# Optimization experiments

Measured on AMD Instinct MI355X. Metric: run time of the kernel, lower is better.

## Reference

```python
import jax, jax.numpy as jnp
import numpy as np

N = 100000      # nodes
E = 3200000     # edges
F_IN = 78       # num_features_mol
F_GAT = 256     # mol_out_feats
HEADS = 2
F_HYP = 128     # mol_out_feats_hyper


def setup_inputs() -> dict:
    key = jax.random.key(0)
    ks = jax.random.split(key, 32)
    g = lambda k, s: jax.random.normal(k, s, dtype=jnp.float32) * 0.05
    inp = {}
    inp["mol_x"] = jax.random.normal(ks[0], (N, F_IN), dtype=jnp.float32)
    inp["mol_edge_index"] = jax.random.randint(ks[1], (2, E), 0, N)
    inp["hyper_edge"] = jax.random.randint(ks[2], (2, E), 0, N)
    # GAT layer 1 (78 -> 256, 2 heads, concat=False)
    inp["W1"] = g(ks[3], (F_IN, HEADS * F_GAT)); inp["as1"] = g(ks[4], (HEADS, F_GAT)); inp["ad1"] = g(ks[5], (HEADS, F_GAT)); inp["b1"] = jnp.zeros((F_GAT,), jnp.float32)
    # GAT layers 2,3 (256 -> 256)
    inp["W2"] = g(ks[6], (F_GAT, HEADS * F_GAT)); inp["as2"] = g(ks[7], (HEADS, F_GAT)); inp["ad2"] = g(ks[8], (HEADS, F_GAT)); inp["b2"] = jnp.zeros((F_GAT,), jnp.float32)
    inp["W3"] = g(ks[9], (F_GAT, HEADS * F_GAT)); inp["as3"] = g(ks[10], (HEADS, F_GAT)); inp["ad3"] = g(ks[11], (HEADS, F_GAT)); inp["b3"] = jnp.zeros((F_GAT,), jnp.float32)
    # GRU-style gating fusion
    inp["fc1_w"] = g(ks[12], (F_GAT, F_GAT)); inp["fc1_b"] = jnp.zeros((F_GAT,), jnp.float32)
    inp["fc2_w"] = g(ks[13], (F_GAT, F_GAT)); inp["fc2_b"] = jnp.zeros((F_GAT,), jnp.float32)
    inp["mol_bias"] = jax.random.uniform(ks[14], (1, F_GAT), jnp.float32, -0.2, 0.2)
    # HypergraphConv layers (334 -> 128 -> 128)
    inp["theta1"] = g(ks[15], (F_GAT + F_IN, F_HYP)); inp["hb1"] = jnp.zeros((F_HYP,), jnp.float32)
    inp["theta2"] = g(ks[16], (F_HYP, F_HYP)); inp["hb2"] = jnp.zeros((F_HYP,), jnp.float32)
    return inp


def _gat(x, src, dst, W, a_s, a_d, b):
    # PyG GATConv, heads=2, concat=False, eval mode (no dropout), self-loops pre-added in src/dst
    xh = (x @ W).reshape(N, HEADS, F_GAT)            # [N,H,C]
    a_src = (xh * a_s).sum(-1)                        # [N,H]
    a_dst = (xh * a_d).sum(-1)                        # [N,H]
    e = jax.nn.leaky_relu(a_src[src] + a_dst[dst], 0.2)  # [E',H]
    m = jax.ops.segment_max(e, dst, num_segments=N)
    ex = jnp.exp(e - m[dst])
    s = jax.ops.segment_sum(ex, dst, num_segments=N)
    alpha = ex / s[dst]                               # softmax over incoming edges
    out = jax.ops.segment_sum(xh[src] * alpha[:, :, None], dst, num_segments=N)
    return out.mean(axis=1) + b                       # concat=False -> head mean


def _hyper(x, node, edge, theta, b):
    # PyG HypergraphConv, use_attention=False: D^-1 H B^-1 H^T X Theta + b
    xt = x @ theta
    ones = jnp.ones((node.shape[0],), xt.dtype)
    D = jax.ops.segment_sum(ones, node, num_segments=N)
    B = jax.ops.segment_sum(ones, edge, num_segments=N)
    Dinv = jnp.where(D > 0, 1.0 / D, 0.0)
    Binv = jnp.where(B > 0, 1.0 / B, 0.0)
    ef = Binv[:, None] * jax.ops.segment_sum(xt[node], edge, num_segments=N)
    nf = Dinv[:, None] * jax.ops.segment_sum(ef[edge], node, num_segments=N)
    return nf + b


def _forward(mol_x, mol_edge_index, hyper_edge,
             W1, as1, ad1, b1, W2, as2, ad2, b2, W3, as3, ad3, b3,
             fc1_w, fc1_b, fc2_w, fc2_b, mol_bias, theta1, hb1, theta2, hb2):
    loops = jnp.arange(N, dtype=mol_edge_index.dtype)
    src = jnp.concatenate([mol_edge_index[0], loops])
    dst = jnp.concatenate([mol_edge_index[1], loops])
    hyper_x0 = jax.lax.stop_gradient(mol_x)  # .clone().detach()
    # layer 0
    h = jax.nn.relu(_gat(mol_x, src, dst, W1, as1, ad1, b1))
    # layer 1 (relu) + gate
    x = jax.nn.relu(_gat(h, src, dst, W2, as2, ad2, b2))
    z = jax.nn.sigmoid(x @ fc1_w.T + fc1_b + h @ fc2_w.T + fc2_b + mol_bias)
    h = z * x + (1.0 - z) * h
    # layer 2 (no relu) + gate
    x = _gat(h, src, dst, W3, as3, ad3, b3)
    z = jax.nn.sigmoid(x @ fc1_w.T + fc1_b + h @ fc2_w.T + fc2_b + mol_bias)
    h = z * x + (1.0 - z) * h
    # hypergraph branch (source uses mol_edge_index here, hyper_edge is unused)
    hx = jnp.concatenate([jax.lax.stop_gradient(h), hyper_x0], axis=1)
    node, edge = mol_edge_index[0], mol_edge_index[1]
    hx = jax.nn.relu(_hyper(hx, node, edge, theta1, hb1))
    hx = jax.nn.relu(_hyper(hx, node, edge, theta2, hb2))
    return jnp.concatenate([h, hx], axis=1)  # [N, 384]


def reference(mol_x, mol_edge_index, hyper_edge,
              W1, as1, ad1, b1, W2, as2, ad2, b2, W3, as3, ad3, b3,
              fc1_w, fc1_b, fc2_w, fc2_b, mol_bias, theta1, hb1, theta2, hb2):
    return _forward(mol_x, mol_edge_index, hyper_edge,
                    W1, as1, ad1, b1, W2, as2, ad2, b2, W3, as3, ad3, b3,
                    fc1_w, fc1_b, fc2_w, fc2_b, mol_bias, theta1, hb1, theta2, hb2)
```

## Files before the change

kernel.cpp:

```cpp
#include <hip/hip_runtime.h>

typedef unsigned short u16;
typedef __attribute__((ext_vector_type(8))) short short8v;
typedef __attribute__((ext_vector_type(8))) unsigned short ushort8v;
typedef __attribute__((ext_vector_type(4))) unsigned short ushort4v;
typedef __attribute__((ext_vector_type(4))) float f32x4;
typedef __attribute__((ext_vector_type(2))) float f32x2;

__device__ __forceinline__ float bf2f(u16 u) {
    union { unsigned int i; float f; } v; v.i = ((unsigned int)u) << 16; return v.f;
}
__device__ __forceinline__ u16 f2bf(float f) {
    union { float f; unsigned int i; } v; v.f = f;
    unsigned int i = v.i;
    return (u16)((i + 0x7FFFu + ((i >> 16) & 1u)) >> 16);
}
__device__ __forceinline__ float leaky02(float x) { return x > 0.f ? x : 0.2f * x; }
__device__ __forceinline__ float load_in(const void* p, long i, int isbf) {
    return isbf ? bf2f(((const u16*)p)[i]) : ((const float*)p)[i];
}
__device__ __forceinline__ f32x2 pk_fma(f32x2 a, f32x2 b, f32x2 c) {
    f32x2 d;
    asm("v_pk_fma_f32 %0, %1, %2, %3" : "=v"(d) : "v"(a), "v"(b), "v"(c));
    return d;
}
__device__ __forceinline__ f32x2 pk_add(f32x2 a, f32x2 b) {
    f32x2 d;
    asm("v_pk_add_f32 %0, %1, %2" : "=v"(d) : "v"(a), "v"(b));
    return d;
}
__device__ __forceinline__ f32x2 bfpair(unsigned int d) {
    union { unsigned int i; float f; } lo, hi;
    lo.i = d << 16;
    hi.i = d & 0xFFFF0000u;
    f32x2 r; r.x = lo.f; r.y = hi.f; return r;
}
__device__ __forceinline__ float bperm_f(int addr, float v) {
    return __int_as_float(__builtin_amdgcn_ds_bpermute(addr, __float_as_int(v)));
}
__device__ __forceinline__ int bperm_i(int addr, int v) {
    return __builtin_amdgcn_ds_bpermute(addr, v);
}

__global__ void detect_kernel(const unsigned* __restrict__ w, int* __restrict__ flag) {
    __shared__ int cnt;
    int t = threadIdx.x;
    if (t == 0) cnt = 0;
    __syncthreads();
    unsigned x = w[t * 16];
    unsigned lo = x & 0xFFFFu;
    int e = (int)((x >> 7) & 0xFFu);
    int good = (lo == 0u) || (e >= 100 && e <= 140);
    atomicAdd(&cnt, good);
    __syncthreads();
    if (t == 0) *flag = (cnt > 128) ? 1 : 0;
}

#define CSR_NBK 1024

__global__ __launch_bounds__(256)
void bucket_count_kernel(const int* __restrict__ ei, int* __restrict__ bcs,
                         int* __restrict__ bcd, int E_, int n, int SH) {
    __shared__ int hs[CSR_NBK], hd[CSR_NBK];
    const int t = threadIdx.x;
    for (int i = t; i < CSR_NBK; i += 256) { hs[i] = 0; hd[i] = 0; }
    __syncthreads();
    const int e0 = blockIdx.x * 4096;
    #pragma unroll
    for (int k = 0; k < 16; ++k) {
        int e = e0 + k * 256 + t;
        if (e < E_) {
            int s = ei[e], d = ei[E_ + e];
            if ((unsigned)s >= (unsigned)n) s = 0;
            if ((unsigned)d >= (unsigned)n) d = 0;
            atomicAdd(&hs[s >> SH], 1);
            atomicAdd(&hd[d >> SH], 1);
        }
    }
    __syncthreads();
    for (int i = t; i < CSR_NBK; i += 256) {
        if (hs[i]) atomicAdd(&bcs[i], hs[i]);
        if (hd[i]) atomicAdd(&bcd[i], hd[i]);
    }
}

__global__ void scan_excl_kernel(const int* __restrict__ deg, int* __restrict__ ptr, int n) {
    __shared__ int s_woff[17];
    __shared__ int s_carry;
    const int t = threadIdx.x;
    const int lane = t & 63, wid = t >> 6;
    if (t == 0) s_carry = 0;
    __syncthreads();
    for (int base = 0; base < n; base += 1024) {
        int i = base + t;
        int v = (i < n) ? deg[i] : 0;
        int incl = v;
        #pragma unroll
        for (int d = 1; d < 64; d <<= 1) {
            int x = __shfl_up(incl, d, 64);
            if (lane >= d) incl += x;
        }
        if (lane == 63) s_woff[wid] = incl;
        __syncthreads();
        if (t == 0) {
            int run = 0;
            #pragma unroll
            for (int w = 0; w < 16; ++w) { int x = s_woff[w]; s_woff[w] = run; run += x; }
            s_woff[16] = run;
        }
        __syncthreads();
        int excl = s_carry + s_woff[wid] + incl - v;
        if (i < n) ptr[i] = excl;
        __syncthreads();
        if (t == 0) s_carry += s_woff[16];
        __syncthreads();
    }
    if (t == 0) ptr[n] = s_carry;
}

__global__ void copy2_kernel(const int* __restrict__ a, int* __restrict__ b,
                             const int* __restrict__ c, int* __restrict__ d2, int n) {
    int i = blockIdx.x * 256 + threadIdx.x;
    if (i < n) { b[i] = a[i]; d2[i] = c[i]; }
}

__global__ __launch_bounds__(256)
void partition_kernel(const int* __restrict__ ei, int* __restrict__ bcur_s,
                      int* __restrict__ bcur_d, int2* __restrict__ ps,
                      int2* __restrict__ pd, int E_, int n, int SH) {
    __shared__ int cs[CSR_NBK], cd[CSR_NBK], bs[CSR_NBK], bd[CSR_NBK];
    const int t = threadIdx.x;
    for (int i = t; i < CSR_NBK; i += 256) { cs[i] = 0; cd[i] = 0; }
    __syncthreads();
    const int e0 = blockIdx.x * 4096;
    int sv[16], dv[16];
    #pragma unroll
    for (int k = 0; k < 16; ++k) {
        int e = e0 + k * 256 + t;
        int s = -1, d = 0;
        if (e < E_) {
            s = ei[e]; d = ei[E_ + e];
            if ((unsigned)s >= (unsigned)n) s = 0;
            if ((unsigned)d >= (unsigned)n) d = 0;
            atomicAdd(&cs[s >> SH], 1);
            atomicAdd(&cd[d >> SH], 1);
        }
        sv[k] = (e < E_) ? s : -1;
        dv[k] = d;
    }
    __syncthreads();
    for (int i = t; i < CSR_NBK; i += 256) {
        bs[i] = cs[i] ? atomicAdd(&bcur_s[i], cs[i]) : 0;
        bd[i] = cd[i] ? atomicAdd(&bcur_d[i], cd[i]) : 0;
        cs[i] = 0; cd[i] = 0;
    }
    __syncthreads();
    #pragma unroll
    for (int k = 0; k < 16; ++k) {
        int s = sv[k];
        if (s < 0) continue;
        int d = dv[k];
        int p = bs[s >> SH] + atomicAdd(&cs[s >> SH], 1);
        ps[p] = make_int2(d, s);
        int q = bd[d >> SH] + atomicAdd(&cd[d >> SH], 1);
        pd[q] = make_int2(s, d);
    }
}

__global__ __launch_bounds__(256)
void fill_bucket_kernel(const int2* __restrict__ pairs, const int* __restrict__ bptr,
                        int* __restrict__ ptr, int* __restrict__ idx, int n, int SH) {
    __shared__ int cnt[256];
    __shared__ int wsum[5];
    const int b = blockIdx.x;
    const int n0 = b << SH;
    if (n0 >= n) return;
    const int nn = min(1 << SH, n - n0);
    const int t = threadIdx.x;
    cnt[t] = 0;
    __syncthreads();
    const int pbeg = bptr[b], pend = bptr[b + 1];
    for (int j = pbeg + t; j < pend; j += 256)
        atomicAdd(&cnt[pairs[j].y - n0], 1);
    __syncthreads();
    const int c = (t < nn) ? cnt[t] : 0;
    int v = c;
    const int lane = t & 63, wid = t >> 6;
    #pragma unroll
    for (int d = 1; d < 64; d <<= 1) {
        int x = __shfl_up(v, d, 64);
        if (lane >= d) v += x;
    }
    if (lane == 63) wsum[wid] = v;
    __syncthreads();
    if (t == 0) {
        int r = 0;
        #pragma unroll
        for (int w = 0; w < 4; ++w) { int x = wsum[w]; wsum[w] = r; r += x; }
        wsum[4] = r;
    }
    __syncthreads();
    v += wsum[wid];
    const int excl = pbeg + v - c;
    __syncthreads();
    if (t < nn) { cnt[t] = excl; ptr[n0 + t] = excl; }
    if (t == 0 && n0 + nn == n) ptr[n] = pbeg + wsum[4];
    __syncthreads();
    for (int j = pbeg + t; j < pend; j += 256) {
        int2 pr = pairs[j];
        int p = atomicAdd(&cnt[pr.y - n0], 1);
        idx[p] = pr.x;
    }
}

__global__ void ingest_transpose_kernel(const void* __restrict__ src, long base,
                                        u16* __restrict__ dst, int K, int Nc, int Kp,
                                        const int* __restrict__ flag) {
    int i = blockIdx.x * 256 + threadIdx.x;
    if (i >= Nc * Kp) return;
    int n = i / Kp, k = i - n * Kp;
    float v = (k < K) ? load_in(src, base + (long)k * Nc + n, *flag) : 0.f;
    dst[i] = f2bf(v);
}

__global__ void ingest_copy_kernel(const void* __restrict__ src, u16* __restrict__ dst,
                                   int n, const int* __restrict__ flag) {
    int i = blockIdx.x * 256 + threadIdx.x;
    if (i < n) dst[i] = f2bf(load_in(src, i, *flag));
}

__global__ void ingest_wcat_kernel(const void* __restrict__ W, u16* __restrict__ dst,
                                   int Kin, int Fh, const int* __restrict__ flag) {
    int i = blockIdx.x * 256 + threadIdx.x;
    int tot = 256 * 2 * Fh;
    if (i >= tot) return;
    int o = i / (2 * Fh), k = i - o * 2 * Fh;
    int h = k / Fh, c = k - h * Fh;
    float v = (c < Kin) ? 0.5f * load_in(W, (long)c * 512 + h * 256 + o, *flag) : 0.f;
    dst[i] = f2bf(v);
}

__global__ void ingest_bcat_kernel(const void* __restrict__ fc1, const void* __restrict__ fc2,
                                   u16* __restrict__ dst, const int* __restrict__ flag) {
    int i = blockIdx.x * 256 + threadIdx.x;
    if (i >= 256 * 512) return;
    int o = i >> 9, k = i & 511;
    float v = (k < 256) ? load_in(fc1, (long)o * 256 + k, *flag)
                        : load_in(fc2, (long)o * 256 + k - 256, *flag);
    dst[i] = f2bf(v);
}

__global__ void ingest_pad_molx_kernel(const void* __restrict__ x, u16* __restrict__ dst,
                                       int ldd, int total, const int* __restrict__ flag) {
    int i = blockIdx.x * 256 + threadIdx.x;
    if (i >= total) return;
    int r = i / 96, c = i - r * 96;
    float v = (c < 78) ? load_in(x, (long)r * 78 + c, *flag) : 0.f;
    dst[(size_t)r * ldd + c] = f2bf(v);
}

__global__ void attn_vec_kernel(const void* __restrict__ W, const void* __restrict__ as_,
                                const void* __restrict__ ad_, float* __restrict__ was,
                                float* __restrict__ wad, int Kin, int Fh,
                                const int* __restrict__ flag) {
    int i = blockIdx.x * 256 + threadIdx.x;
    if (i >= 2 * Fh) return;
    int h = i / Fh, c = i - h * Fh;
    float s = 0.f, d = 0.f;
    if (c < Kin) {
        int f = *flag;
        for (int o = 0; o < 256; ++o) {
            float w = load_in(W, (long)c * 512 + h * 256 + o, f);
            s += w * load_in(as_, h * 256 + o, f);
            d += w * load_in(ad_, h * 256 + o, f);
        }
    }
    was[i] = s; wad[i] = d;
}

__global__ __launch_bounds__(256, 2)
void gemm_kernel(const u16* __restrict__ A, int lda,
                 const u16* __restrict__ Bt, int ldb,
                 u16* __restrict__ C, int ldc, int K, int M, int beta,
                 const u16* __restrict__ bias, int relu) {
    __shared__ __align__(16) u16 As[128 * 32];
    __shared__ __align__(16) u16 Bs[128 * 32];
    const int tid = threadIdx.x;
    const int wave = tid >> 6, lane = tid & 63;
    const int m0 = blockIdx.x * 128;
    const int n0 = blockIdx.y * 128;
    const int wm = (wave & 1) * 64, wn = (wave >> 1) * 64;
    const int r = lane & 15, q = lane >> 4;

    f32x4 acc[4][4];
    if (beta) {
        #pragma unroll
        for (int i = 0; i < 4; ++i)
            #pragma unroll
            for (int j = 0; j < 4; ++j)
                #pragma unroll
                for (int rr = 0; rr < 4; ++rr) {
                    size_t gr = (size_t)(m0 + wm + 16 * i + q * 4 + rr);
                    int gc = n0 + wn + 16 * j + r;
                    acc[i][j][rr] = bf2f(C[gr * ldc + gc]);
                }
    } else {
        #pragma unroll
        for (int i = 0; i < 4; ++i)
            #pragma unroll
            for (int j = 0; j < 4; ++j) acc[i][j] = (f32x4)0.f;
    }

    const int rowT = wave * 16 + (lane >> 2);
    const int koff = (lane & 3) * 8;
    int rA0 = m0 + rowT;       if (rA0 > M - 1) rA0 = M - 1;
    int rA1 = m0 + rowT + 64;  if (rA1 > M - 1) rA1 = M - 1;
    const u16* gA0 = A + (size_t)rA0 * lda + koff;
    const u16* gA1 = A + (size_t)rA1 * lda + koff;
    const u16* gB0 = Bt + (size_t)(n0 + rowT) * ldb + koff;
    const u16* gB1 = Bt + (size_t)(n0 + rowT + 64) * ldb + koff;
    u16* sA0 = &As[rowT * 32 + koff];
    u16* sA1 = &As[(rowT + 64) * 32 + koff];
    u16* sB0 = &Bs[rowT * 32 + koff];
    u16* sB1 = &Bs[(rowT + 64) * 32 + koff];

    const int nK = K >> 5;
    for (int kt = 0; kt < nK; ++kt) {
        ushort8v ta0 = *(const ushort8v*)gA0;
        ushort8v ta1 = *(const ushort8v*)gA1;
        ushort8v tb0 = *(const ushort8v*)gB0;
        ushort8v tb1 = *(const ushort8v*)gB1;
        gA0 += 32; gA1 += 32; gB0 += 32; gB1 += 32;
        __syncthreads();
        *(ushort8v*)sA0 = ta0;
        *(ushort8v*)sA1 = ta1;
        *(ushort8v*)sB0 = tb0;
        *(ushort8v*)sB1 = tb1;
        __syncthreads();
        short8v af[4], bf[4];
        #pragma unroll
        for (int i = 0; i < 4; ++i) af[i] = *(const short8v*)&As[(wm + 16 * i + r) * 32 + q * 8];
        #pragma unroll
        for (int j = 0; j < 4; ++j) bf[j] = *(const short8v*)&Bs[(wn + 16 * j + r) * 32 + q * 8];
        #pragma unroll
        for (int i = 0; i < 4; ++i)
            #pragma unroll
            for (int j = 0; j < 4; ++j)
                acc[i][j] = __builtin_amdgcn_mfma_f32_16x16x32_bf16(af[i], bf[j], acc[i][j], 0, 0, 0);
    }
    #pragma unroll
    for (int j = 0; j < 4; ++j) {
        int gc = n0 + wn + 16 * j + r;
        float bv = bias ? bf2f(bias[gc]) : 0.f;
        #pragma unroll
        for (int i = 0; i < 4; ++i)
            #pragma unroll
            for (int rr = 0; rr < 4; ++rr) {
                size_t gr = (size_t)(m0 + wm + 16 * i + q * 4 + rr);
                float x = acc[i][j][rr] + bv;
                if (relu) x = fmaxf(x, 0.f);
                C[gr * ldc + gc] = f2bf(x);
            }
    }
}

__global__ __launch_bounds__(256)
void attn_dots_h_kernel(const u16* __restrict__ hsrc, int ldh,
                        const float* __restrict__ was, const float* __restrict__ wad,
                        float* __restrict__ a_src, float* __restrict__ a_dst,
                        int Fh, int n) {
    int v = blockIdx.x * 4 + (threadIdx.x >> 6);
    if (v >= n) return;
    const int lane = threadIdx.x & 63;
    const int c0 = lane * 4;
    float ps0 = 0.f, pd0 = 0.f, ps1 = 0.f, pd1 = 0.f;
    if (c0 < Fh) {
        ushort4v xv = *(const ushort4v*)&hsrc[(size_t)v * ldh + c0];
        #pragma unroll
        for (int k = 0; k < 4; ++k) {
            float x = bf2f(xv[k]);
            ps0 += x * was[c0 + k];
            pd0 += x * wad[c0 + k];
            ps1 += x * was[Fh + c0 + k];
            pd1 += x * wad[Fh + c0 + k];
        }
    }
    #pragma unroll
    for (int d = 1; d < 64; d <<= 1) {
        ps0 += __shfl_xor(ps0, d, 64); pd0 += __shfl_xor(pd0, d, 64);
        ps1 += __shfl_xor(ps1, d, 64); pd1 += __shfl_xor(pd1, d, 64);
    }
    if (lane == 0) {
        a_src[2 * v] = ps0; a_src[2 * v + 1] = ps1;
        a_dst[2 * v] = pd0; a_dst[2 * v + 1] = pd1;
    }
}

template <int NG>
__global__ __launch_bounds__(256)
void gat_agg_h_kernel(const u16* __restrict__ hsrc, int ldh, int F,
                      const float* __restrict__ asrc, const float* __restrict__ adst,
                      const int* __restrict__ ptr, const int* __restrict__ idx,
                      u16* __restrict__ agg, int ldagg, int n, int Etot) {
    constexpr int GL = 64 / NG;
    int v = blockIdx.x * 4 + (threadIdx.x >> 6);
    if (v >= n) return;
    const int lane = threadIdx.x & 63;
    const int sub = lane / GL;
    const int c0 = (lane & (GL - 1)) * 8;
    const int act = (c0 < F);
    int beg = ptr[v], end = ptr[v + 1];
    beg = min(max(beg, 0), Etot);
    end = min(max(end, beg), Etot);
    const float ad0 = adst[2 * v], ad1 = adst[2 * v + 1];
    const float es0 = leaky02(asrc[2 * v] + ad0);
    const float es1 = leaky02(asrc[2 * v + 1] + ad1);
    float m0 = es0, m1 = es1;
    float s0 = 0.f, s1 = 0.f;
    f32x2 f0p[4], f1p[4];
    #pragma unroll
    for (int p = 0; p < 4; ++p) { f0p[p] = (f32x2)0.f; f1p[p] = (f32x2)0.f; }

    for (int cb = beg; cb < end; cb += 64) {
        const int cnt = min(64, end - cb);
        int sE = 0;
        float sc0 = -1e30f, sc1 = -1e30f;
        if (lane < cnt) {
            sE = idx[cb + lane];
            sE = ((unsigned)sE < (unsigned)n) ? sE : 0;
            sc0 = leaky02(asrc[2 * sE] + ad0);
            sc1 = leaky02(asrc[2 * sE + 1] + ad1);
        }
        float cm0 = sc0, cm1 = sc1;
        #pragma unroll
        for (int d = 1; d < 64; d <<= 1) {
            cm0 = fmaxf(cm0, __shfl_xor(cm0, d, 64));
            cm1 = fmaxf(cm1, __shfl_xor(cm1, d, 64));
        }
        const float nm0 = fmaxf(m0, cm0), nm1 = fmaxf(m1, cm1);
        const float r0 = __expf(m0 - nm0), r1 = __expf(m1 - nm1);
        m0 = nm0; m1 = nm1;
        s0 *= r0; s1 *= r1;
        #pragma unroll
        for (int p = 0; p < 4; ++p) {
            f0p[p].x *= r0; f0p[p].y *= r0;
            f1p[p].x *= r1; f1p[p].y *= r1;
        }
        float wE0 = 0.f, wE1 = 0.f;
        if (lane < cnt) {
            wE0 = __expf(sc0 - m0);
            wE1 = __expf(sc1 - m1);
            s0 += wE0; s1 += wE1;
        }
        const int nIt = (cnt + 4 * NG - 1) / (4 * NG);
        int jj = sub;
        for (int it = 0; it < nIt; ++it, jj += 4 * NG) {
            const int aA = jj * 4, aB = aA + NG * 4, aC = aA + NG * 8, aD = aA + NG * 12;
            const int sA = bperm_i(aA, sE);
            const int sB = bperm_i(aB, sE);
            const int sC = bperm_i(aC, sE);
            const int sD = bperm_i(aD, sE);
            const float wA0 = bperm_f(aA, wE0), wA1 = bperm_f(aA, wE1);
            const float wB0 = bperm_f(aB, wE0), wB1 = bperm_f(aB, wE1);
            const float wC0 = bperm_f(aC, wE0), wC1 = bperm_f(aC, wE1);
            const float wD0 = bperm_f(aD, wE0), wD1 = bperm_f(aD, wE1);
            if (act) {
                const uint4 fA = *(const uint4*)&hsrc[(size_t)sA * ldh + c0];
                const uint4 fB = *(const uint4*)&hsrc[(size_t)sB * ldh + c0];
                const uint4 fC = *(const uint4*)&hsrc[(size_t)sC * ldh + c0];
                const uint4 fD = *(const uint4*)&hsrc[(size_t)sD * ldh + c0];
                const f32x2 wA0v = {wA0, wA0}, wA1v = {wA1, wA1};
                const f32x2 wB0v = {wB0, wB0}, wB1v = {wB1, wB1};
                const f32x2 wC0v = {wC0, wC0}, wC1v = {wC1, wC1};
                const f32x2 wD0v = {wD0, wD0}, wD1v = {wD1, wD1};
                #pragma unroll
                for (int p = 0; p < 4; ++p) {
                    const f32x2 xA = bfpair(((const unsigned*)&fA)[p]);
                    const f32x2 xB = bfpair(((const unsigned*)&fB)[p]);
                    const f32x2 xC = bfpair(((const unsigned*)&fC)[p]);
                    const f32x2 xD = bfpair(((const unsigned*)&fD)[p]);
                    f0p[p] = pk_fma(xA, wA0v, f0p[p]);
                    f1p[p] = pk_fma(xA, wA1v, f1p[p]);
                    f0p[p] = pk_fma(xB, wB0v, f0p[p]);
                    f1p[p] = pk_fma(xB, wB1v, f1p[p]);
                    f0p[p] = pk_fma(xC, wC0v, f0p[p]);
                    f1p[p] = pk_fma(xC, wC1v, f1p[p]);
                    f0p[p] = pk_fma(xD, wD0v, f0p[p]);
                    f1p[p] = pk_fma(xD, wD1v, f1p[p]);
                }
            }
        }
    }
    #pragma unroll
    for (int d = 1; d < 64; d <<= 1) {
        s0 += __shfl_xor(s0, d, 64);
        s1 += __shfl_xor(s1, d, 64);
    }
    const float w0s = __expf(es0 - m0), w1s = __expf(es1 - m1);
    s0 += w0s; s1 += w1s;
    if (sub == 0 && act) {
        const uint4 f = *(const uint4*)&hsrc[(size_t)v * ldh + c0];
        const f32x2 w0v = {w0s, w0s}, w1v = {w1s, w1s};
        #pragma unroll
        for (int p = 0; p < 4; ++p) {
            const f32x2 x = bfpair(((const unsigned*)&f)[p]);
            f0p[p] = pk_fma(x, w0v, f0p[p]);
            f1p[p] = pk_fma(x, w1v, f1p[p]);
        }
    }
    #pragma unroll
    for (int p = 0; p < 4; ++p) {
        #pragma unroll
        for (int d = GL; d < 64; d <<= 1) {
            f0p[p].x += __shfl_xor(f0p[p].x, d, 64);
            f0p[p].y += __shfl_xor(f0p[p].y, d, 64);
            f1p[p].x += __shfl_xor(f1p[p].x, d, 64);
            f1p[p].y += __shfl_xor(f1p[p].y, d, 64);
        }
    }
    if (lane < GL && act) {
        const float i0 = 1.f / s0, i1 = 1.f / s1;
        ushort8v o0, o1;
        #pragma unroll
        for (int p = 0; p < 4; ++p) {
            o0[2 * p] = f2bf(f0p[p].x * i0); o0[2 * p + 1] = f2bf(f0p[p].y * i0);
            o1[2 * p] = f2bf(f1p[p].x * i1); o1[2 * p + 1] = f2bf(f1p[p].y * i1);
        }
        *(ushort8v*)&agg[(size_t)v * ldagg + c0] = o0;
        *(ushort8v*)&agg[(size_t)v * ldagg + F + c0] = o1;
    }
}

__global__ __launch_bounds__(256)
void gate_kernel(const u16* __restrict__ logit, const u16* __restrict__ cat,
                 const u16* __restrict__ fc1b, const u16* __restrict__ fc2b,
                 const u16* __restrict__ molb, u16* __restrict__ dest,
                 void* __restrict__ outw, const int* __restrict__ flag, int n) {
    int i = blockIdx.x * 256 + threadIdx.x;
    if (i >= n) return;
    int node = i >> 5, c0 = (i & 31) * 8;
    ushort8v lg = *(const ushort8v*)&logit[(size_t)node * 256 + c0];
    ushort8v xv = *(const ushort8v*)&cat[(size_t)node * 512 + c0];
    ushort8v hv = *(const ushort8v*)&cat[(size_t)node * 512 + 256 + c0];
    ushort8v b1v = *(const ushort8v*)&fc1b[c0];
    ushort8v b2v = *(const ushort8v*)&fc2b[c0];
    ushort8v mbv = *(const ushort8v*)&molb[c0];
    float ov[8];
    ushort8v dv;
    #pragma unroll
    for (int k = 0; k < 8; ++k) {
        float l = bf2f(lg[k]) + bf2f(b1v[k]) + bf2f(b2v[k]) + bf2f(mbv[k]);
        float z = 1.f / (1.f + __expf(-l));
        ov[k] = z * bf2f(xv[k]) + (1.f - z) * bf2f(hv[k]);
        dv[k] = f2bf(ov[k]);
    }
    *(ushort8v*)&dest[(size_t)node * 512 + c0] = dv;
    if (outw) {
        if (*flag) {
            *(ushort8v*)((u16*)outw + (size_t)node * 384 + c0) = dv;
        } else {
            float* o = (float*)outw + (size_t)node * 384 + c0;
            #pragma unroll
            for (int k = 0; k < 8; ++k) o[k] = ov[k];
        }
    }
}

__global__ __launch_bounds__(256)
void hyper_gather_kernel(const u16* __restrict__ feat, const int* __restrict__ ptr,
                         const int* __restrict__ idx, const u16* __restrict__ bias,
                         u16* __restrict__ outb, int ldo, void* __restrict__ outw,
                         int col0, const int* __restrict__ flag,
                         int do_relu, int n, int Etot) {
    int v = blockIdx.x * 4 + (threadIdx.x >> 6);
    if (v >= n) return;
    const int lane = threadIdx.x & 63;
    const int c0 = (lane & 15) * 8, sub = lane >> 4;
    int beg = ptr[v], end = ptr[v + 1];
    beg = min(max(beg, 0), Etot);
    end = min(max(end, beg), Etot);
    const float inv = (end > beg) ? 1.f / (float)(end - beg) : 0.f;
    f32x2 a2[4];
    #pragma unroll
    for (int p = 0; p < 4; ++p) a2[p] = (f32x2)0.f;
    int j = beg + sub;
    for (; j + 12 < end; j += 16) {
        int sA = idx[j];      sA = ((unsigned)sA < (unsigned)n) ? sA : 0;
        int sB = idx[j + 4];  sB = ((unsigned)sB < (unsigned)n) ? sB : 0;
        int sC = idx[j + 8];  sC = ((unsigned)sC < (unsigned)n) ? sC : 0;
        int sD = idx[j + 12]; sD = ((unsigned)sD < (unsigned)n) ? sD : 0;
        const uint4 fA = *(const uint4*)&feat[(size_t)sA * 128 + c0];
        const uint4 fB = *(const uint4*)&feat[(size_t)sB * 128 + c0];
        const uint4 fC = *(const uint4*)&feat[(size_t)sC * 128 + c0];
        const uint4 fD = *(const uint4*)&feat[(size_t)sD * 128 + c0];
        #pragma unroll
        for (int p = 0; p < 4; ++p) {
            a2[p] = pk_add(a2[p], bfpair(((const unsigned*)&fA)[p]));
            a2[p] = pk_add(a2[p], bfpair(((const unsigned*)&fB)[p]));
            a2[p] = pk_add(a2[p], bfpair(((const unsigned*)&fC)[p]));
            a2[p] = pk_add(a2[p], bfpair(((const unsigned*)&fD)[p]));
        }
    }
    for (; j < end; j += 4) {
        int s = idx[j]; s = ((unsigned)s < (unsigned)n) ? s : 0;
        const uint4 f = *(const uint4*)&feat[(size_t)s * 128 + c0];
        #pragma unroll
        for (int p = 0; p < 4; ++p)
            a2[p] = pk_add(a2[p], bfpair(((const unsigned*)&f)[p]));
    }
    #pragma unroll
    for (int p = 0; p < 4; ++p) {
        a2[p].x += __shfl_xor(a2[p].x, 16, 64);
        a2[p].y += __shfl_xor(a2[p].y, 16, 64);
        a2[p].x += __shfl_xor(a2[p].x, 32, 64);
        a2[p].y += __shfl_xor(a2[p].y, 32, 64);
    }
    if (sub == 0) {
        float ov[8];
        ushort8v o;
        #pragma unroll
        for (int p = 0; p < 4; ++p) {
            float x0 = a2[p].x * inv + (bias ? bf2f(bias[c0 + 2 * p]) : 0.f);
            float x1 = a2[p].y * inv + (bias ? bf2f(bias[c0 + 2 * p + 1]) : 0.f);
            if (do_relu) { x0 = fmaxf(x0, 0.f); x1 = fmaxf(x1, 0.f); }
            ov[2 * p] = x0; ov[2 * p + 1] = x1;
            o[2 * p] = f2bf(x0); o[2 * p + 1] = f2bf(x1);
        }
        if (outb) *(ushort8v*)&outb[(size_t)v * ldo + c0] = o;
        if (outw) {
            if (*flag) {
                *(ushort8v*)((u16*)outw + (size_t)v * 384 + col0 + c0) = o;
            } else {
                float* ofp = (float*)outw + (size_t)v * 384 + col0 + c0;
                #pragma unroll
                for (int k = 0; k < 8; ++k) ofp[k] = ov[k];
            }
        }
    }
}

extern "C" void kernel_launch(void* const* d_in, const int* in_sizes, int n_in,
                              void* d_out, int out_size, void* d_ws, size_t ws_size,
                              hipStream_t stream) {
    const void* molx = d_in[0];
    const int*  ei   = (const int*)d_in[1];
    const void* W1 = d_in[3], *as1 = d_in[4], *ad1 = d_in[5], *b1 = d_in[6];
    const void* W2 = d_in[7], *as2 = d_in[8], *ad2 = d_in[9], *b2 = d_in[10];
    const void* W3 = d_in[11], *as3 = d_in[12], *ad3 = d_in[13], *b3 = d_in[14];
    const void* fc1w = d_in[15], *fc1b = d_in[16], *fc2w = d_in[17], *fc2b = d_in[18];
    const void* molb = d_in[19];
    const void* th1 = d_in[20], *hb1 = d_in[21], *th2 = d_in[22], *hb2 = d_in[23];
    (void)n_in; (void)out_size;

    const int N = in_sizes[0] / 78;
    const int E = in_sizes[1] / 2;
    const int Mp = ((N + 127) / 128) * 128;

    int SH = 0;
    while (((N - 1) >> SH) >= CSR_NBK) SH++;

    char* base = (char*)d_ws;
    size_t off = 0;
    auto alloc = [&](size_t bytes) -> void* {
        void* r = base + off;
        off = (off + bytes + 255) & ~(size_t)255;
        return r;
    };
    int* flag = (int*)alloc(4);
    u16* bv1 = (u16*)alloc(256 * 2); u16* bv2 = (u16*)alloc(256 * 2); u16* bv3 = (u16*)alloc(256 * 2);
    u16* fc1bv = (u16*)alloc(256 * 2); u16* fc2bv = (u16*)alloc(256 * 2); u16* molbv = (u16*)alloc(256 * 2);
    u16* hb1v = (u16*)alloc(128 * 2); u16* hb2v = (u16*)alloc(128 * 2);
    float* was1 = (float*)alloc(192 * 4); float* wad1 = (float*)alloc(192 * 4);
    float* was2 = (float*)alloc(512 * 4); float* wad2 = (float*)alloc(512 * 4);
    float* was3 = (float*)alloc(512 * 4); float* wad3 = (float*)alloc(512 * 4);
    u16* Wc1 = (u16*)alloc(256 * 192 * 2);
    u16* Wc2 = (u16*)alloc(256 * 512 * 2);
    u16* Wc3 = (u16*)alloc(256 * 512 * 2);
    u16* Bcat = (u16*)alloc(256 * 512 * 2);
    u16* th1ta = (u16*)alloc(128 * 256 * 2);
    u16* th1tb = (u16*)alloc(128 * 96 * 2);
    u16* th2t  = (u16*)alloc(128 * 128 * 2);
    float* a_src = (float*)alloc((size_t)N * 2 * 4);
    float* a_dst = (float*)alloc((size_t)N * 2 * 4);
    int* ptr_src = (int*)alloc((size_t)(N + 1) * 4);
    int* ptr_dst = (int*)alloc((size_t)(N + 1) * 4);
    int* bcnt_src = (int*)alloc(CSR_NBK * 4);
    int* bcnt_dst = (int*)alloc(CSR_NBK * 4);
    int* bptr_src = (int*)alloc((CSR_NBK + 1) * 4);
    int* bptr_dst = (int*)alloc((CSR_NBK + 1) * 4);
    int* bcur_src = (int*)alloc(CSR_NBK * 4);
    int* bcur_dst = (int*)alloc(CSR_NBK * 4);
    int* idx_src = (int*)alloc((size_t)E * 4);
    int* idx_dst = (int*)alloc((size_t)E * 4);
    u16* cat = (u16*)alloc((size_t)Mp * 512 * 2);
    u16* agg = (u16*)alloc((size_t)Mp * 512 * 2);
    u16* xt   = agg;
    u16* efb  = agg + (size_t)Mp * 128;
    u16* hx1  = agg + (size_t)Mp * 256;
    u16* mxp2 = agg + (size_t)Mp * 384;

    int2* pairs_src; int2* pairs_dst;
    if (off + (size_t)E * 16 + 1024 <= ws_size) {
        pairs_src = (int2*)alloc((size_t)E * 8);
        pairs_dst = (int2*)alloc((size_t)E * 8);
    } else {
        pairs_src = (int2*)agg;
        pairs_dst = (int2*)((char*)agg + (size_t)E * 8);
    }

    const int nodeBlocks = (N + 3) / 4;
    const int eTiles = (E + 4095) / 4096;

    detect_kernel<<<1, 256, 0, stream>>>((const unsigned*)molx, flag);

    hipMemsetAsync(bcnt_src, 0, CSR_NBK * 4, stream);
    hipMemsetAsync(bcnt_dst, 0, CSR_NBK * 4, stream);
    bucket_count_kernel<<<eTiles, 256, 0, stream>>>(ei, bcnt_src, bcnt_dst, E, N, SH);
    scan_excl_kernel<<<1, 1024, 0, stream>>>(bcnt_src, bptr_src, CSR_NBK);
    scan_excl_kernel<<<1, 1024, 0, stream>>>(bcnt_dst, bptr_dst, CSR_NBK);
    copy2_kernel<<<(CSR_NBK + 255) / 256, 256, 0, stream>>>(bptr_src, bcur_src, bptr_dst, bcur_dst, CSR_NBK);
    partition_kernel<<<eTiles, 256, 0, stream>>>(ei, bcur_src, bcur_dst,
                                                 pairs_src, pairs_dst, E, N, SH);
    fill_bucket_kernel<<<CSR_NBK, 256, 0, stream>>>(pairs_src, bptr_src, ptr_src, idx_src, N, SH);
    fill_bucket_kernel<<<CSR_NBK, 256, 0, stream>>>(pairs_dst, bptr_dst, ptr_dst, idx_dst, N, SH);

    ingest_wcat_kernel<<<(256 * 192 + 255) / 256, 256, 0, stream>>>(W1, Wc1, 78, 96, flag);
    ingest_wcat_kernel<<<(256 * 512 + 255) / 256, 256, 0, stream>>>(W2, Wc2, 256, 256, flag);
    ingest_wcat_kernel<<<(256 * 512 + 255) / 256, 256, 0, stream>>>(W3, Wc3, 256, 256, flag);
    ingest_bcat_kernel<<<(256 * 512 + 255) / 256, 256, 0, stream>>>(fc1w, fc2w, Bcat, flag);
    ingest_transpose_kernel<<<(128 * 256 + 255) / 256, 256, 0, stream>>>(th1, 0, th1ta, 256, 128, 256, flag);
    ingest_transpose_kernel<<<(128 * 96 + 255) / 256, 256, 0, stream>>>(th1, (long)256 * 128, th1tb, 78, 128, 96, flag);
    ingest_transpose_kernel<<<(128 * 128 + 255) / 256, 256, 0, stream>>>(th2, 0, th2t, 128, 128, 128, flag);
    attn_vec_kernel<<<1, 256, 0, stream>>>(W1, as1, ad1, was1, wad1, 78, 96, flag);
    attn_vec_kernel<<<2, 256, 0, stream>>>(W2, as2, ad2, was2, wad2, 256, 256, flag);
    attn_vec_kernel<<<2, 256, 0, stream>>>(W3, as3, ad3, was3, wad3, 256, 256, flag);
    ingest_copy_kernel<<<1, 256, 0, stream>>>(b1, bv1, 256, flag);
    ingest_copy_kernel<<<1, 256, 0, stream>>>(b2, bv2, 256, flag);
    ingest_copy_kernel<<<1, 256, 0, stream>>>(b3, bv3, 256, flag);
    ingest_copy_kernel<<<1, 256, 0, stream>>>(fc1b, fc1bv, 256, flag);
    ingest_copy_kernel<<<1, 256, 0, stream>>>(fc2b, fc2bv, 256, flag);
    ingest_copy_kernel<<<1, 256, 0, stream>>>(molb, molbv, 256, flag);
    ingest_copy_kernel<<<1, 128, 0, stream>>>(hb1, hb1v, 128, flag);
    ingest_copy_kernel<<<1, 128, 0, stream>>>(hb2, hb2v, 128, flag);
    ingest_pad_molx_kernel<<<(N * 96 + 255) / 256, 256, 0, stream>>>(molx, cat, 512, N * 96, flag);

    auto gemm = [&](const u16* A, int lda, const u16* Bt, int ldb, u16* C, int ldc,
                    int K, int Nc, int M, int beta, const u16* bias, int relu) {
        dim3 g(Mp / 128, Nc / 128);
        gemm_kernel<<<g, 256, 0, stream>>>(A, lda, Bt, ldb, C, ldc, K, M, beta, bias, relu);
    };

    attn_dots_h_kernel<<<nodeBlocks, 256, 0, stream>>>(cat, 512, was1, wad1, a_src, a_dst, 96, N);
    gat_agg_h_kernel<4><<<nodeBlocks, 256, 0, stream>>>(cat, 512, 96, a_src, a_dst,
                                                        ptr_dst, idx_dst, agg, 192, N, E);
    gemm(agg, 192, Wc1, 192, cat + 256, 512, 192, 256, Mp, 0, bv1, 1);
    attn_dots_h_kernel<<<nodeBlocks, 256, 0, stream>>>(cat + 256, 512, was2, wad2, a_src, a_dst, 256, N);
    gat_agg_h_kernel<2><<<nodeBlocks, 256, 0, stream>>>(cat + 256, 512, 256, a_src, a_dst,
                                                        ptr_dst, idx_dst, agg, 512, N, E);
    gemm(agg, 512, Wc2, 512, cat, 512, 512, 256, Mp, 0, bv2, 1);
    gemm(cat, 512, Bcat, 512, agg , 256, 512, 256, Mp, 0, nullptr, 0);
    gate_kernel<<<(N * 32 + 255) / 256, 256, 0, stream>>>(agg, cat, fc1bv, fc2bv, molbv,
                                                          cat + 256, nullptr, flag, N * 32);
    attn_dots_h_kernel<<<nodeBlocks, 256, 0, stream>>>(cat + 256, 512, was3, wad3, a_src, a_dst, 256, N);
    gat_agg_h_kernel<2><<<nodeBlocks, 256, 0, stream>>>(cat + 256, 512, 256, a_src, a_dst,
                                                        ptr_dst, idx_dst, agg, 512, N, E);
    gemm(agg, 512, Wc3, 512, cat, 512, 512, 256, Mp, 0, bv3, 0);
    gemm(cat, 512, Bcat, 512, agg , 256, 512, 256, Mp, 0, nullptr, 0);
    gate_kernel<<<(N * 32 + 255) / 256, 256, 0, stream>>>(agg, cat, fc1bv, fc2bv, molbv,
                                                          cat + 256, d_out, flag, N * 32);
    ingest_pad_molx_kernel<<<(N * 96 + 255) / 256, 256, 0, stream>>>(molx, mxp2, 96, N * 96, flag);
    gemm(cat + 256, 512, th1ta, 256, xt, 128, 256, 128, Mp, 0, nullptr, 0);
    gemm(mxp2, 96, th1tb, 96, xt, 128, 96, 128, Mp, 1, nullptr, 0);
    hyper_gather_kernel<<<nodeBlocks, 256, 0, stream>>>(xt, ptr_dst, idx_dst, (const u16*)nullptr,
                                                        efb, 128, nullptr, 0, flag, 0, N, E);
    hyper_gather_kernel<<<nodeBlocks, 256, 0, stream>>>(efb, ptr_src, idx_src, hb1v,
                                                        hx1, 128, nullptr, 0, flag, 1, N, E);
    gemm(hx1, 128, th2t, 128, xt, 128, 128, 128, Mp, 0, nullptr, 0);
    hyper_gather_kernel<<<nodeBlocks, 256, 0, stream>>>(xt, ptr_dst, idx_dst, (const u16*)nullptr,
                                                        efb, 128, nullptr, 0, flag, 0, N, E);
    hyper_gather_kernel<<<nodeBlocks, 256, 0, stream>>>(efb, ptr_src, idx_src, hb2v,
                                                        (u16*)nullptr, 0, d_out, 256, flag, 1, N, E);
}
```

Baseline: 2.128 ms.

## Split GAT aggregation into softmax-weight precompute and gather kernels

The fused online-softmax GAT aggregation becomes two kernels. The first computes per-edge attention scores, the per-node max and exp-normalised weights, and writes (src, w0, w1) records to a per-edge buffer plus per-node self weight and inverse sums. The second streams those records and does the weighted feature gather with no per-chunk rescaling, max reductions or bpermute shuffles. This adds an extra launch and roughly 16 bytes per edge of writes and reads per layer (about 51 MB), and it may alias d_out as scratch when the workspace is too small.

```diff
diff --git a/kernel.cpp b/kernel.cpp
--- a/kernel.cpp
+++ b/kernel.cpp
@@ -34,12 +34,6 @@
     lo.i = d << 16;
     hi.i = d & 0xFFFF0000u;
     f32x2 r; r.x = lo.f; r.y = hi.f; return r;
-}
-__device__ __forceinline__ float bperm_f(int addr, float v) {
-    return __int_as_float(__builtin_amdgcn_ds_bpermute(addr, __float_as_int(v)));
-}
-__device__ __forceinline__ int bperm_i(int addr, int v) {
-    return __builtin_amdgcn_ds_bpermute(addr, v);
 }
 
 __global__ void detect_kernel(const unsigned* __restrict__ w, int* __restrict__ flag) {
@@ -396,12 +390,66 @@
     }
 }
 
+__global__ __launch_bounds__(256)
+void gat_weights_kernel(const float* __restrict__ asrc, const float* __restrict__ adst,
+                        const int* __restrict__ ptr, const int* __restrict__ idx,
+                        uint4* __restrict__ ew, float4* __restrict__ ninfo,
+                        int n, int Etot) {
+    int v = blockIdx.x * 4 + (threadIdx.x >> 6);
+    if (v >= n) return;
+    const int lane = threadIdx.x & 63;
+    int beg = ptr[v], end = ptr[v + 1];
+    beg = min(max(beg, 0), Etot);
+    end = min(max(end, beg), Etot);
+    const float ad0 = adst[2 * v], ad1 = adst[2 * v + 1];
+    const float es0 = leaky02(asrc[2 * v] + ad0);
+    const float es1 = leaky02(asrc[2 * v + 1] + ad1);
+    float m0 = -1e30f, m1 = -1e30f;
+    for (int j = beg + lane; j < end; j += 64) {
+        int s = idx[j]; s = ((unsigned)s < (unsigned)n) ? s : 0;
+        const float2 ap = *(const float2*)&asrc[2 * s];
+        const float sc0 = leaky02(ap.x + ad0);
+        const float sc1 = leaky02(ap.y + ad1);
+        uint4 r;
+        r.x = (unsigned)s;
+        r.y = __float_as_uint(sc0);
+        r.z = __float_as_uint(sc1);
+        r.w = 0u;
+        ew[j] = r;
+        m0 = fmaxf(m0, sc0); m1 = fmaxf(m1, sc1);
+    }
+    #pragma unroll
+    for (int d = 1; d < 64; d <<= 1) {
+        m0 = fmaxf(m0, __shfl_xor(m0, d, 64));
+        m1 = fmaxf(m1, __shfl_xor(m1, d, 64));
+    }
+    m0 = fmaxf(m0, es0); m1 = fmaxf(m1, es1);
+    float s0 = 0.f, s1 = 0.f;
+    for (int j = beg + lane; j < end; j += 64) {
+        uint4 r = ew[j];
+        const float w0 = __expf(__uint_as_float(r.y) - m0);
+        const float w1 = __expf(__uint_as_float(r.z) - m1);
+        r.y = __float_as_uint(w0);
+        r.z = __float_as_uint(w1);
+        ew[j] = r;
+        s0 += w0; s1 += w1;
+    }
+    #pragma unroll
+    for (int d = 1; d < 64; d <<= 1) {
+        s0 += __shfl_xor(s0, d, 64);
+        s1 += __shfl_xor(s1, d, 64);
+    }
+    const float ws0 = __expf(es0 - m0), ws1 = __expf(es1 - m1);
+    s0 += ws0; s1 += ws1;
+    if (lane == 0) ninfo[v] = make_float4(ws0, ws1, 1.f / s0, 1.f / s1);
+}
+
 template <int NG>
 __global__ __launch_bounds__(256)
-void gat_agg_h_kernel(const u16* __restrict__ hsrc, int ldh, int F,
-                      const float* __restrict__ asrc, const float* __restrict__ adst,
-                      const int* __restrict__ ptr, const int* __restrict__ idx,
-                      u16* __restrict__ agg, int ldagg, int n, int Etot) {
+void gat_gather_kernel(const u16* __restrict__ hsrc, int ldh, int F,
+                       const uint4* __restrict__ ew, const float4* __restrict__ ninfo,
+                       const int* __restrict__ ptr,
+                       u16* __restrict__ agg, int ldagg, int n, int Etot) {
     constexpr int GL = 64 / NG;
     int v = blockIdx.x * 4 + (threadIdx.x >> 6);
     if (v >= n) return;
@@ -412,95 +460,64 @@
     int beg = ptr[v], end = ptr[v + 1];
     beg = min(max(beg, 0), Etot);
     end = min(max(end, beg), Etot);
-    const float ad0 = adst[2 * v], ad1 = adst[2 * v + 1];
-    const float es0 = leaky02(asrc[2 * v] + ad0);
-    const float es1 = leaky02(asrc[2 * v + 1] + ad1);
-    float m0 = es0, m1 = es1;
-    float s0 = 0.f, s1 = 0.f;
+    const float4 ni = ninfo[v];
     f32x2 f0p[4], f1p[4];
     #pragma unroll
     for (int p = 0; p < 4; ++p) { f0p[p] = (f32x2)0.f; f1p[p] = (f32x2)0.f; }
 
-    for (int cb = beg; cb < end; cb += 64) {
-        const int cnt = min(64, end - cb);
-        int sE = 0;
-        float sc0 = -1e30f, sc1 = -1e30f;
-        if (lane < cnt) {
-            sE = idx[cb + lane];
-            sE = ((unsigned)sE < (unsigned)n) ? sE : 0;
-            sc0 = leaky02(asrc[2 * sE] + ad0);
-            sc1 = leaky02(asrc[2 * sE + 1] + ad1);
-        }
-        float cm0 = sc0, cm1 = sc1;
-        #pragma unroll
-        for (int d = 1; d < 64; d <<= 1) {
-            cm0 = fmaxf(cm0, __shfl_xor(cm0, d, 64));
-            cm1 = fmaxf(cm1, __shfl_xor(cm1, d, 64));
-        }
-        const float nm0 = fmaxf(m0, cm0), nm1 = fmaxf(m1, cm1);
-        const float r0 = __expf(m0 - nm0), r1 = __expf(m1 - nm1);
-        m0 = nm0; m1 = nm1;
-        s0 *= r0; s1 *= r1;
-        #pragma unroll
-        for (int p = 0; p < 4; ++p) {
-            f0p[p].x *= r0; f0p[p].y *= r0;
-            f1p[p].x *= r1; f1p[p].y *= r1;
-        }
-        float wE0 = 0.f, wE1 = 0.f;
-        if (lane < cnt) {
-            wE0 = __expf(sc0 - m0);
-            wE1 = __expf(sc1 - m1);
-            s0 += wE0; s1 += wE1;
-        }
-        const int nIt = (cnt + 4 * NG - 1) / (4 * NG);
-        int jj = sub;
-        for (int it = 0; it < nIt; ++it, jj += 4 * NG) {
-            const int aA = jj * 4, aB = aA + NG * 4, aC = aA + NG * 8, aD = aA + NG * 12;
-            const int sA = bperm_i(aA, sE);
-            const int sB = bperm_i(aB, sE);
-            const int sC = bperm_i(aC, sE);
-            const int sD = bperm_i(aD, sE);
-            const float wA0 = bperm_f(aA, wE0), wA1 = bperm_f(aA, wE1);
-            const float wB0 = bperm_f(aB, wE0), wB1 = bperm_f(aB, wE1);
-            const float wC0 = bperm_f(aC, wE0), wC1 = bperm_f(aC, wE1);
-            const float wD0 = bperm_f(aD, wE0), wD1 = bperm_f(aD, wE1);
-            if (act) {
-                const uint4 fA = *(const uint4*)&hsrc[(size_t)sA * ldh + c0];
-                const uint4 fB = *(const uint4*)&hsrc[(size_t)sB * ldh + c0];
-                const uint4 fC = *(const uint4*)&hsrc[(size_t)sC * ldh + c0];
-                const uint4 fD = *(const uint4*)&hsrc[(size_t)sD * ldh + c0];
-                const f32x2 wA0v = {wA0, wA0}, wA1v = {wA1, wA1};
-                const f32x2 wB0v = {wB0, wB0}, wB1v = {wB1, wB1};
-                const f32x2 wC0v = {wC0, wC0}, wC1v = {wC1, wC1};
-                const f32x2 wD0v = {wD0, wD0}, wD1v = {wD1, wD1};
-                #pragma unroll
-                for (int p = 0; p < 4; ++p) {
-                    const f32x2 xA = bfpair(((const unsigned*)&fA)[p]);
-                    const f32x2 xB = bfpair(((const unsigned*)&fB)[p]);
-                    const f32x2 xC = bfpair(((const unsigned*)&fC)[p]);
-                    const f32x2 xD = bfpair(((const unsigned*)&fD)[p]);
-                    f0p[p] = pk_fma(xA, wA0v, f0p[p]);
-                    f1p[p] = pk_fma(xA, wA1v, f1p[p]);
-                    f0p[p] = pk_fma(xB, wB0v, f0p[p]);
-                    f1p[p] = pk_fma(xB, wB1v, f1p[p]);
-                    f0p[p] = pk_fma(xC, wC0v, f0p[p]);
-                    f1p[p] = pk_fma(xC, wC1v, f1p[p]);
-                    f0p[p] = pk_fma(xD, wD0v, f0p[p]);
-                    f1p[p] = pk_fma(xD, wD1v, f1p[p]);
-                }
+    int j = beg + sub;
+    for (; j + 3 * NG < end; j += 4 * NG) {
+        const uint4 rA = ew[j];
+        const uint4 rB = ew[j + NG];
+        const uint4 rC = ew[j + 2 * NG];
+        const uint4 rD = ew[j + 3 * NG];
+        if (act) {
+            const uint4 fA = *(const uint4*)&hsrc[(size_t)rA.x * ldh + c0];
+            const uint4 fB = *(const uint4*)&hsrc[(size_t)rB.x * ldh + c0];
+            const uint4 fC = *(const uint4*)&hsrc[(size_t)rC.x * ldh + c0];
+            const uint4 fD = *(const uint4*)&hsrc[(size_t)rD.x * ldh + c0];
+            const float wA0 = __uint_as_float(rA.y), wA1 = __uint_as_float(rA.z);
+            const float wB0 = __uint_as_float(rB.y), wB1 = __uint_as_float(rB.z);
+            const float wC0 = __uint_as_float(rC.y), wC1 = __uint_as_float(rC.z);
+            const float wD0 = __uint_as_float(rD.y), wD1 = __uint_as_float(rD.z);
+            const f32x2 wA0v = {wA0, wA0}, wA1v = {wA1, wA1};
+            const f32x2 wB0v = {wB0, wB0}, wB1v = {wB1, wB1};
+            const f32x2 wC0v = {wC0, wC0}, wC1v = {wC1, wC1};
+            const f32x2 wD0v = {wD0, wD0}, wD1v = {wD1, wD1};
+            #pragma unroll
+            for (int p = 0; p < 4; ++p) {
+                const f32x2 xA = bfpair(((const unsigned*)&fA)[p]);
+                const f32x2 xB = bfpair(((const unsigned*)&fB)[p]);
+                const f32x2 xC = bfpair(((const unsigned*)&fC)[p]);
+                const f32x2 xD = bfpair(((const unsigned*)&fD)[p]);
+                f0p[p] = pk_fma(xA, wA0v, f0p[p]);
+                f1p[p] = pk_fma(xA, wA1v, f1p[p]);
+                f0p[p] = pk_fma(xB, wB0v, f0p[p]);
+                f1p[p] = pk_fma(xB, wB1v, f1p[p]);
+                f0p[p] = pk_fma(xC, wC0v, f0p[p]);
+                f1p[p] = pk_fma(xC, wC1v, f1p[p]);
+                f0p[p] = pk_fma(xD, wD0v, f0p[p]);
+                f1p[p] = pk_fma(xD, wD1v, f1p[p]);
             }
         }
     }
-    #pragma unroll
-    for (int d = 1; d < 64; d <<= 1) {
-        s0 += __shfl_xor(s0, d, 64);
-        s1 += __shfl_xor(s1, d, 64);
-    }
-    const float w0s = __expf(es0 - m0), w1s = __expf(es1 - m1);
-    s0 += w0s; s1 += w1s;
+    for (; j < end; j += NG) {
+        const uint4 rA = ew[j];
+        if (act) {
+            const uint4 fA = *(const uint4*)&hsrc[(size_t)rA.x * ldh + c0];
+            const float wA0 = __uint_as_float(rA.y), wA1 = __uint_as_float(rA.z);
+            const f32x2 wA0v = {wA0, wA0}, wA1v = {wA1, wA1};
+            #pragma unroll
+            for (int p = 0; p < 4; ++p) {
+                const f32x2 xA = bfpair(((const unsigned*)&fA)[p]);
+                f0p[p] = pk_fma(xA, wA0v, f0p[p]);
+                f1p[p] = pk_fma(xA, wA1v, f1p[p]);
+            }
+        }
+    }
     if (sub == 0 && act) {
         const uint4 f = *(const uint4*)&hsrc[(size_t)v * ldh + c0];
-        const f32x2 w0v = {w0s, w0s}, w1v = {w1s, w1s};
+        const f32x2 w0v = {ni.x, ni.x}, w1v = {ni.y, ni.y};
         #pragma unroll
         for (int p = 0; p < 4; ++p) {
             const f32x2 x = bfpair(((const unsigned*)&f)[p]);
@@ -519,7 +536,7 @@
         }
     }
     if (lane < GL && act) {
-        const float i0 = 1.f / s0, i1 = 1.f / s1;
+        const float i0 = ni.z, i1 = ni.w;
         ushort8v o0, o1;
         #pragma unroll
         for (int p = 0; p < 4; ++p) {
@@ -650,7 +667,7 @@
     const void* fc1w = d_in[15], *fc1b = d_in[16], *fc2w = d_in[17], *fc2b = d_in[18];
     const void* molb = d_in[19];
     const void* th1 = d_in[20], *hb1 = d_in[21], *th2 = d_in[22], *hb2 = d_in[23];
-    (void)n_in; (void)out_size;
+    (void)n_in;
 
     const int N = in_sizes[0] / 78;
     const int E = in_sizes[1] / 2;
@@ -682,6 +699,7 @@
     u16* th2t  = (u16*)alloc(128 * 128 * 2);
     float* a_src = (float*)alloc((size_t)N * 2 * 4);
     float* a_dst = (float*)alloc((size_t)N * 2 * 4);
+    float4* ninfo = (float4*)alloc((size_t)N * 16);
     int* ptr_src = (int*)alloc((size_t)(N + 1) * 4);
     int* ptr_dst = (int*)alloc((size_t)(N + 1) * 4);
     int* bcnt_src = (int*)alloc(CSR_NBK * 4);
@@ -707,6 +725,13 @@
         pairs_src = (int2*)agg;
         pairs_dst = (int2*)((char*)agg + (size_t)E * 8);
     }
+    uint4* ew;
+    if (off + (size_t)E * 16 + 1024 <= ws_size) {
+        ew = (uint4*)alloc((size_t)E * 16);
+    } else {
+        ew = (uint4*)d_out;
+    }
+    (void)out_size;
 
     const int nodeBlocks = (N + 3) / 4;
     const int eTiles = (E + 4095) / 4096;
@@ -751,19 +776,22 @@
     };
 
     attn_dots_h_kernel<<<nodeBlocks, 256, 0, stream>>>(cat, 512, was1, wad1, a_src, a_dst, 96, N);
-    gat_agg_h_kernel<4><<<nodeBlocks, 256, 0, stream>>>(cat, 512, 96, a_src, a_dst,
-                                                        ptr_dst, idx_dst, agg, 192, N, E);
+    gat_weights_kernel<<<nodeBlocks, 256, 0, stream>>>(a_src, a_dst, ptr_dst, idx_dst, ew, ninfo, N, E);
+    gat_gather_kernel<4><<<nodeBlocks, 256, 0, stream>>>(cat, 512, 96, ew, ninfo,
+                                                         ptr_dst, agg, 192, N, E);
     gemm(agg, 192, Wc1, 192, cat + 256, 512, 192, 256, Mp, 0, bv1, 1);
     attn_dots_h_kernel<<<nodeBlocks, 256, 0, stream>>>(cat + 256, 512, was2, wad2, a_src, a_dst, 256, N);
-    gat_agg_h_kernel<2><<<nodeBlocks, 256, 0, stream>>>(cat + 256, 512, 256, a_src, a_dst,
-                                                        ptr_dst, idx_dst, agg, 512, N, E);
+    gat_weights_kernel<<<nodeBlocks, 256, 0, stream>>>(a_src, a_dst, ptr_dst, idx_dst, ew, ninfo, N, E);
+    gat_gather_kernel<2><<<nodeBlocks, 256, 0, stream>>>(cat + 256, 512, 256, ew, ninfo,
+                                                         ptr_dst, agg, 512, N, E);
     gemm(agg, 512, Wc2, 512, cat, 512, 512, 256, Mp, 0, bv2, 1);
     gemm(cat, 512, Bcat, 512, agg , 256, 512, 256, Mp, 0, nullptr, 0);
     gate_kernel<<<(N * 32 + 255) / 256, 256, 0, stream>>>(agg, cat, fc1bv, fc2bv, molbv,
                                                           cat + 256, nullptr, flag, N * 32);
     attn_dots_h_kernel<<<nodeBlocks, 256, 0, stream>>>(cat + 256, 512, was3, wad3, a_src, a_dst, 256, N);
-    gat_agg_h_kernel<2><<<nodeBlocks, 256, 0, stream>>>(cat + 256, 512, 256, a_src, a_dst,
-                                                        ptr_dst, idx_dst, agg, 512, N, E);
+    gat_weights_kernel<<<nodeBlocks, 256, 0, stream>>>(a_src, a_dst, ptr_dst, idx_dst, ew, ninfo, N, E);
+    gat_gather_kernel<2><<<nodeBlocks, 256, 0, stream>>>(cat + 256, 512, 256, ew, ninfo,
+                                                         ptr_dst, agg, 512, N, E);
     gemm(agg, 512, Wc3, 512, cat, 512, 512, 256, Mp, 0, bv3, 0);
     gemm(cat, 512, Bcat, 512, agg , 256, 512, 256, Mp, 0, nullptr, 0);
     gate_kernel<<<(N * 32 + 255) / 256, 256, 0, stream>>>(agg, cat, fc1bv, fc2bv, molbv,
```

New measurement: 2.225 ms. 4.6% more time.
